# Performance work log

Hardware: AMD Instinct MI355X
Metric: run time of the kernel (lower is better)

Reference implementation:

```python
import jax, jax.numpy as jnp
import numpy as np

N = 100_000       # nodes
E = 1_600_000     # edges
G = 128           # graphs in batch
RAW_ND, RAW_ED = 9, 3
ND, ED, H = 16, 2, 32  # node_dim, edge_dim, GAT hidden (heads=1)


def _p(key, shape, scale=0.1):
    return jax.random.normal(key, shape, dtype=jnp.float32) * scale


def setup_inputs() -> dict:
    key = jax.random.key(0)
    ks = jax.random.split(key, 32)
    inp = {
        "node_feat": jax.random.normal(ks[0], (N, RAW_ND), dtype=jnp.float32),
        "edge_index": jax.random.randint(ks[1], (2, E), 0, N, dtype=jnp.int64)
        if jax.config.jax_enable_x64 else jax.random.randint(ks[1], (2, E), 0, N).astype(jnp.int32),
        "edge_attr": jax.random.normal(ks[2], (E, RAW_ED), dtype=jnp.float32),
        "batch": jnp.sort(jax.random.randint(ks[3], (N,), 0, G)).astype(jnp.int32),
        # encoders
        "W_ne": _p(ks[4], (RAW_ND, ND)), "b_ne": jnp.zeros((ND,), jnp.float32),
        "W_ee": _p(ks[5], (RAW_ED, ED)), "b_ee": jnp.zeros((ED,), jnp.float32),
        # readout
        "W_l3": _p(ks[6], (3 * H, 1)), "b_l3": jnp.zeros((1,), jnp.float32),
    }
    dims_in = [ND, H, H]
    for i in range(3):
        k = jax.random.split(ks[7 + i], 6)
        inp[f"W{i}"] = _p(k[0], (dims_in[i], H))
        inp[f"as{i}"] = _p(k[1], (H,))
        inp[f"ad{i}"] = _p(k[2], (H,))
        inp[f"We{i}"] = _p(k[3], (ED, H))
        inp[f"ae{i}"] = _p(k[4], (H,))
        inp[f"bb{i}"] = jnp.zeros((H,), jnp.float32)
    return inp


def _segment_softmax(logits, seg, num_segments):
    m = jax.ops.segment_max(logits, seg, num_segments=num_segments)
    m = jnp.where(jnp.isfinite(m), m, 0.0)
    e = jnp.exp(logits - m[seg])
    s = jax.ops.segment_sum(e, seg, num_segments=num_segments)
    return e / (s[seg] + 1e-16)


def _gat(x, src, dst, ef, W, a_s, a_d, We, a_e, b):
    # PyG GATConv, heads=1, negative_slope=0.2
    h = x @ W                                   # [N', H]
    a_src = h @ a_s                             # [N']
    a_dst = h @ a_d
    a_edge = (ef @ We) @ a_e                    # [E']
    logits = jax.nn.leaky_relu(a_src[src] + a_dst[dst] + a_edge, 0.2)
    att = _segment_softmax(logits, dst, h.shape[0])
    out = jax.ops.segment_sum(h[src] * att[:, None], dst, num_segments=h.shape[0])
    return out + b


def reference(node_feat, edge_index, edge_attr, batch,
              W_ne, b_ne, W_ee, b_ee, W_l3, b_l3,
              W0, as0, ad0, We0, ae0, bb0,
              W1, as1, ad1, We1, ae1, bb1,
              W2, as2, ad2, We2, ae2, bb2):
    n = node_feat.shape[0]
    x = node_feat @ W_ne + b_ne                 # NodeEncoder -> [N,16]
    ef = edge_attr @ W_ee + b_ee                # EdgeEncoder -> [E,2]
    # add_self_loops=True with fill_value='mean' (PyG default when edge_dim set)
    loop = jnp.arange(n, dtype=edge_index.dtype)
    src = jnp.concatenate([edge_index[0], loop])
    dst = jnp.concatenate([edge_index[1], loop])
    ef_fill = jnp.broadcast_to(ef.mean(axis=0), (n, ef.shape[1]))
    ef_aug = jnp.concatenate([ef, ef_fill], axis=0)
    x1 = _gat(x, src, dst, ef_aug, W0, as0, ad0, We0, ae0, bb0)
    x2 = _gat(x1, src, dst, ef_aug, W1, as1, ad1, We1, ae1, bb1)
    x3 = _gat(x2, src, dst, ef_aug, W2, as2, ad2, We2, ae2, bb2)
    x_cat = jnp.concatenate([x1, x2, x3], axis=1)  # [N, 96]
    sums = jax.ops.segment_sum(x_cat, batch, num_segments=G)
    cnt = jax.ops.segment_sum(jnp.ones((n,), x_cat.dtype), batch, num_segments=G)
    pooled = sums / jnp.maximum(cnt, 1.0)[:, None]   # global mean pool [G,96]
    return pooled @ W_l3 + b_l3                      # [G,1]
```

## Files before the change

kernel.cpp:

```cpp
#include <hip/hip_runtime.h>
#include <hip/hip_fp16.h>


#define NBUCK_SHIFT 8
#define NBUCK_MAX 512
#define CAP 6144
#define SLF_BIT 0x00800000u

__global__ void k_pre(const int* __restrict__ ei1, int* __restrict__ bucket_cnt,
                      const int* __restrict__ batch, int* __restrict__ bounds,
                      const float* __restrict__ Wne, const float* __restrict__ bne,
                      const float* __restrict__ W0, float* __restrict__ wf,
                      int n, int e, int ep, int nbH) {
    int b = blockIdx.x, t = threadIdx.x;
    if (b < nbH) {
        __shared__ int lh[NBUCK_MAX];
        lh[t] = 0; lh[t + 256] = 0;
        __syncthreads();
        int base = b * 4096;
#pragma unroll
        for (int i = 0; i < 16; ++i) {
            int gid = base + i * 256 + t;
            if (gid < ep) {
                int d = (gid < e) ? ei1[gid] : gid - e;
                atomicAdd(&lh[d >> NBUCK_SHIFT], 1);
            }
        }
        __syncthreads();
        if (lh[t]) atomicAdd(&bucket_cnt[t], lh[t]);
        if (lh[t + 256]) atomicAdd(&bucket_cnt[t + 256], lh[t + 256]);
        return;
    }
    for (int i = t; i < 288; i += 256) {
        int m = i >> 5, j = i & 31;
        float a = 0.f;
        for (int k = 0; k < 16; ++k) a += Wne[m * 16 + k] * W0[k * 32 + j];
        wf[i] = a;
    }
    if (t < 32) {
        float a = 0.f;
        for (int k = 0; k < 16; ++k) a += bne[k] * W0[k * 32 + t];
        wf[288 + t] = a;
    }
    for (int g = t; g <= 128; g += 256) {
        if (g == 128) { bounds[128] = n; continue; }
        int lo = 0, hi = n;
        while (lo < hi) {
            int mid = (lo + hi) >> 1;
            if (batch[mid] < g) lo = mid + 1; else hi = mid;
        }
        bounds[g] = lo;
    }
}

__global__ void k_hproj0(const float* __restrict__ nf, const float* __restrict__ wf,
                         const float* __restrict__ as_, const float* __restrict__ ad_,
                         unsigned int* __restrict__ h2, float* __restrict__ asrc,
                         float* __restrict__ adst, int n) {
    int node = blockIdx.x * 8 + (threadIdx.x >> 5);
    int j = threadIdx.x & 31;
    if (node >= n) return;
    const float* xr = nf + node * 9;
    float acc = wf[288 + j];
#pragma unroll
    for (int m = 0; m < 9; ++m) acc += xr[m] * wf[m * 32 + j];
    float accp = __shfl_down(acc, 1, 32);
    if ((j & 1) == 0) {
        __half2 hh = __floats2half2_rn(acc, accp);
        h2[(size_t)node * 16 + (j >> 1)] = *reinterpret_cast<unsigned int*>(&hh);
    }
    float r1 = acc * as_[j], r2 = acc * ad_[j];
#pragma unroll
    for (int off = 16; off > 0; off >>= 1) {
        r1 += __shfl_xor(r1, off, 32);
        r2 += __shfl_xor(r2, off, 32);
    }
    if (j == 0) { asrc[node] = r1; adst[node] = r2; }
}

__device__ __forceinline__ float2 h2f2u(unsigned int hw) {
    __half2 hh = *reinterpret_cast<__half2*>(&hw);
    return make_float2(__low2float(hh), __high2float(hh));
}

__global__ void k_hproj(const unsigned int* __restrict__ xh, const float* __restrict__ W,
                        const float* __restrict__ as_, const float* __restrict__ ad_,
                        unsigned int* __restrict__ h2, float* __restrict__ asrc,
                        float* __restrict__ adst, int n) {
    __shared__ float sW[1024];
    for (int i = threadIdx.x; i < 1024; i += 256) sW[i] = W[i];
    __syncthreads();
    int node = blockIdx.x * 8 + (threadIdx.x >> 5);
    int j = threadIdx.x & 31;
    if (node >= n) return;
    const unsigned int* xr = xh + (size_t)node * 16;
    float acc = 0.f;
#pragma unroll
    for (int w = 0; w < 16; ++w) {
        float2 f = h2f2u(xr[w]);
        acc += f.x * sW[(2 * w) * 32 + j] + f.y * sW[(2 * w + 1) * 32 + j];
    }
    float accp = __shfl_down(acc, 1, 32);
    if ((j & 1) == 0) {
        __half2 hh = __floats2half2_rn(acc, accp);
        h2[(size_t)node * 16 + (j >> 1)] = *reinterpret_cast<unsigned int*>(&hh);
    }
    float r1 = acc * as_[j], r2 = acc * ad_[j];
#pragma unroll
    for (int off = 16; off > 0; off >>= 1) {
        r1 += __shfl_xor(r1, off, 32);
        r2 += __shfl_xor(r2, off, 32);
    }
    if (j == 0) { asrc[node] = r1; adst[node] = r2; }
}

__global__ void __launch_bounds__(512)
k_scan(const int* __restrict__ bucket_cnt, int* __restrict__ bucket_base,
       int* __restrict__ bcursor, int nbuck, int ep, int* __restrict__ rp, int n) {
    __shared__ int s[512];
    int t = threadIdx.x;
    int v = (t < nbuck) ? bucket_cnt[t] : 0;
    s[t] = v;
    __syncthreads();
    for (int o = 1; o < 512; o <<= 1) {
        int x = (t >= o) ? s[t - o] : 0;
        __syncthreads();
        s[t] += x;
        __syncthreads();
    }
    int ex = s[t] - v;
    if (t < nbuck) { bucket_base[t] = ex; bcursor[t] = ex; }
    if (t == 0) { bucket_base[nbuck] = ep; rp[n] = ep; }
}

__global__ void k_binB(const int* __restrict__ ei0, const int* __restrict__ ei1,
                       const float* __restrict__ ea, const float* __restrict__ We,
                       const float* __restrict__ be, int* __restrict__ bcursor,
                       uint2* __restrict__ st, float2* __restrict__ partial,
                       int e, int ep) {
    __shared__ int lh[NBUCK_MAX], lcur[NBUCK_MAX];
    int t = threadIdx.x;
    lh[t] = 0; lh[t + 256] = 0;
    __syncthreads();
    int base = blockIdx.x * 4096;
    unsigned int sd[16], fh[16];
    int bk[16];
    float w00 = We[0], w10 = We[2], w20 = We[4];
    float w01 = We[1], w11 = We[3], w21 = We[5];
    float b0 = be[0], b1 = be[1];
    float cs0 = 0.f, cs1 = 0.f;
#pragma unroll
    for (int i = 0; i < 16; ++i) {
        int gid = base + i * 256 + t;
        bk[i] = -1;
        if (gid < ep) {
            int s, d;
            if (gid < e) {
                s = ei0[gid]; d = ei1[gid];
                const float* r = ea + (size_t)gid * 3;
                float a0 = r[0], a1 = r[1], a2 = r[2];
                float f0 = a0 * w00 + a1 * w10 + a2 * w20 + b0;
                float f1 = a0 * w01 + a1 * w11 + a2 * w21 + b1;
                cs0 += f0; cs1 += f1;
                sd[i] = ((unsigned int)s << NBUCK_SHIFT) | (unsigned int)(d & 255);
                __half2 hh = __floats2half2_rn(f0, f1);
                fh[i] = *reinterpret_cast<unsigned int*>(&hh);
            } else {
                s = d = gid - e;
                sd[i] = 0x80000000u | ((unsigned int)s << NBUCK_SHIFT)
                      | (unsigned int)(d & 255);
                fh[i] = 0;
            }
            bk[i] = d >> NBUCK_SHIFT;
            atomicAdd(&lh[bk[i]], 1);
        }
    }
#pragma unroll
    for (int off = 32; off > 0; off >>= 1) {
        cs0 += __shfl_xor(cs0, off, 64);
        cs1 += __shfl_xor(cs1, off, 64);
    }
    if ((t & 63) == 0)
        partial[(blockIdx.x << 2) + (t >> 6)] = make_float2(cs0, cs1);
    __syncthreads();
    if (lh[t] > 0) lcur[t] = atomicAdd(&bcursor[t], lh[t]);
    if (lh[t + 256] > 0) lcur[t + 256] = atomicAdd(&bcursor[t + 256], lh[t + 256]);
    __syncthreads();
#pragma unroll
    for (int i = 0; i < 16; ++i) {
        if (bk[i] >= 0) {
            int pos = atomicAdd(&lcur[bk[i]], 1);
            st[pos] = make_uint2(sd[i], fh[i]);
        }
    }
}

__global__ void __launch_bounds__(512)
k_binC(const uint2* __restrict__ st, const int* __restrict__ bucket_base,
       int* __restrict__ rp, uint2* __restrict__ rec, int n, int nbuck,
       const float* __restrict__ We0, const float* __restrict__ ae0,
       const float* __restrict__ We1, const float* __restrict__ ae1,
       const float* __restrict__ We2, const float* __restrict__ ae2,
       const float2* __restrict__ partial, int nw, float einv,
       float* __restrict__ consts) {
    int k = blockIdx.x, t = threadIdx.x;
    if (k == nbuck) {
        __shared__ float r0[512], r1[512];
        float m0 = 0.f, m1 = 0.f;
        for (int i = t; i < nw; i += 512) {
            float2 v = partial[i];
            m0 += v.x; m1 += v.y;
        }
        r0[t] = m0; r1[t] = m1;
        __syncthreads();
        for (int o = 256; o > 0; o >>= 1) {
            if (t < o) { r0[t] += r0[t + o]; r1[t] += r1[t + o]; }
            __syncthreads();
        }
        if (t == 0) {
            float fm0 = r0[0] * einv, fm1 = r1[0] * einv;
            const float* We[3] = {We0, We1, We2};
            const float* ae[3] = {ae0, ae1, ae2};
            for (int l = 0; l < 3; ++l) {
                float c0 = 0.f, c1 = 0.f;
                for (int j = 0; j < 32; ++j) {
                    c0 += We[l][j] * ae[l][j];
                    c1 += We[l][32 + j] * ae[l][j];
                }
                consts[l * 2 + 0] = c0;
                consts[l * 2 + 1] = c1;
                consts[6 + l] = fm0 * c0 + fm1 * c1;
            }
        }
        return;
    }
    __shared__ int nh[256], ns[256];
    __shared__ uint2 rs[CAP];
    int s0 = bucket_base[k], s1 = bucket_base[k + 1];
    int cnt = s1 - s0;
    uint2 lv[12];
    if (t < 256) nh[t] = 0;
    __syncthreads();
#pragma unroll
    for (int u = 0; u < 12; ++u) {
        int i = s0 + u * 512 + t;
        if (i < s1) {
            uint2 v = st[i];
            lv[u] = v;
            atomicAdd(&nh[v.x & 255], 1);
        }
    }
    __syncthreads();
    if (t < 256) ns[t] = nh[t];
    __syncthreads();
    for (int o = 1; o < 256; o <<= 1) {
        int add = 0;
        if (t < 256 && t >= o) add = ns[t - o];
        __syncthreads();
        if (t < 256) ns[t] += add;
        __syncthreads();
    }
    int node0 = k << NBUCK_SHIFT;
    if (t < 256) {
        int startl = ns[t] - nh[t];
        if (node0 + t < n) rp[node0 + t] = s0 + startl;
        nh[t] = startl;
    }
    __syncthreads();
#pragma unroll
    for (int u = 0; u < 12; ++u) {
        int i = s0 + u * 512 + t;
        if (i < s1) {
            uint2 v = lv[u];
            int pos = atomicAdd(&nh[v.x & 255], 1);
            uint2 r = make_uint2(v.x >> NBUCK_SHIFT, v.y);
            if (pos < CAP) rs[pos] = r;
            else rec[s0 + pos] = r;
        }
    }
    __syncthreads();
    int m = cnt < CAP ? cnt : CAP;
    for (int i = t; i < m; i += 512)
        rec[s0 + i] = rs[i];
}

__device__ __forceinline__ void agg_step(const unsigned int* __restrict__ h2,
                                         const uint2* ed, int t, int sub, int woff,
                                         float& a0, float& a1, float& a2, float& a3) {
    uint2 sp = ed[t + sub];
    float p4 = __uint_as_float(sp.y);
    uint2 hv = *reinterpret_cast<const uint2*>(h2 + (((int)sp.x << 4) + woff));
    __half2 hlo = *reinterpret_cast<__half2*>(&hv.x);
    __half2 hhi = *reinterpret_cast<__half2*>(&hv.y);
    a0 = fmaf(__low2float(hlo), p4, a0);
    a1 = fmaf(__high2float(hlo), p4, a1);
    a2 = fmaf(__low2float(hhi), p4, a2);
    a3 = fmaf(__high2float(hhi), p4, a3);
}

template <bool STORE_X>
__global__ void k_agg(const int* __restrict__ rp, const uint2* __restrict__ rec,
                      const float* __restrict__ asrc, const float* __restrict__ adst,
                      const float* __restrict__ consts, const unsigned int* __restrict__ h2,
                      const float* __restrict__ bb, unsigned int* __restrict__ xout,
                      const float* __restrict__ wl3, float* __restrict__ vout,
                      int n, int layer) {
    __shared__ uint2 sed[8][32];
    int g = threadIdx.x >> 5;
    int j = threadIdx.x & 31;
    int sub = j >> 3;
    int q = j & 7;
    int woff = q << 1;
    float c0 = consts[layer * 2], c1 = consts[layer * 2 + 1];
    float loopc = consts[6 + layer];
    float4 bb4 = reinterpret_cast<const float4*>(bb)[q];
    float4 wl34 = reinterpret_cast<const float4*>(wl3)[q];
    uint2* ed = sed[g];
    int stride = gridDim.x * 8;
    for (int node = blockIdx.x * 8 + g; node < n; node += stride) {
        int r0 = rp[node], r1 = rp[node + 1];
        float adn = adst[node];
        float a0 = 0.f, a1 = 0.f, a2 = 0.f, a3 = 0.f, psum = 0.f;
        for (int c = r0; c < r1; c += 32) {
            int i = c + j;
            float pe = 0.f; unsigned int s = 0;
            if (i < r1) {
                unsigned long long rv = *reinterpret_cast<const unsigned long long*>(
                    rec + i);
                unsigned int sx = (unsigned int)rv;
                s = sx & 0x7fffffu;
                unsigned int fv = (unsigned int)(rv >> 32);
                __half2 hh = *reinterpret_cast<__half2*>(&fv);
                float ae = (sx & SLF_BIT) ? loopc
                         : fmaf(__low2float(hh), c0, __high2float(hh) * c1);
                float lg = asrc[s] + adn + ae;
                lg = lg > 0.f ? lg : 0.2f * lg;
                pe = __expf(lg);
            }
            psum += pe;
            ed[j] = make_uint2(s, __float_as_uint(pe));
            int cnt = min(32, r1 - c);
            int t = 0;
            for (; t + 8 <= cnt; t += 8) {
                agg_step(h2, ed, t, sub, woff, a0, a1, a2, a3);
                agg_step(h2, ed, t + 4, sub, woff, a0, a1, a2, a3);
            }
            if (t < cnt) { agg_step(h2, ed, t, sub, woff, a0, a1, a2, a3); t += 4; }
            if (t < cnt) { agg_step(h2, ed, t, sub, woff, a0, a1, a2, a3); }
        }
        a0 += __shfl_xor(a0, 8, 32);  a0 += __shfl_xor(a0, 16, 32);
        a1 += __shfl_xor(a1, 8, 32);  a1 += __shfl_xor(a1, 16, 32);
        a2 += __shfl_xor(a2, 8, 32);  a2 += __shfl_xor(a2, 16, 32);
        a3 += __shfl_xor(a3, 8, 32);  a3 += __shfl_xor(a3, 16, 32);
#pragma unroll
        for (int off = 16; off > 0; off >>= 1) psum += __shfl_xor(psum, off, 32);
        float inv = __builtin_amdgcn_rcpf(psum + 1e-16f);
        float r0v = fmaf(a0, inv, bb4.x);
        float r1v = fmaf(a1, inv, bb4.y);
        float r2v = fmaf(a2, inv, bb4.z);
        float r3v = fmaf(a3, inv, bb4.w);
        if (STORE_X) {
            if (sub == 0) {
                __half2 lo = __floats2half2_rn(r0v, r1v);
                __half2 hi = __floats2half2_rn(r2v, r3v);
                uint2 wv = make_uint2(*reinterpret_cast<unsigned int*>(&lo),
                                      *reinterpret_cast<unsigned int*>(&hi));
                reinterpret_cast<uint2*>(xout)[(size_t)node * 8 + q] = wv;
            }
        }
        float v = r0v * wl34.x + r1v * wl34.y + r2v * wl34.z + r3v * wl34.w;
        v += __shfl_xor(v, 1, 32);
        v += __shfl_xor(v, 2, 32);
        v += __shfl_xor(v, 4, 32);
        if (j == 0) vout[node] = v;
    }
}

__global__ void k_dotv(const float* __restrict__ v0, const float* __restrict__ v1,
                       const float* __restrict__ v2, const int* __restrict__ bounds,
                       const float* __restrict__ bl3, float* __restrict__ out) {
    __shared__ float red[256];
    int g = blockIdx.x, t = threadIdx.x;
    int s0 = bounds[g], s1 = bounds[g + 1];
    float acc = 0.f;
    for (int i = s0 + t; i < s1; i += 256) acc += v0[i] + v1[i] + v2[i];
    red[t] = acc;
    __syncthreads();
    for (int o = 128; o > 0; o >>= 1) {
        if (t < o) red[t] += red[t + o];
        __syncthreads();
    }
    if (t == 0) {
        float c = (float)(s1 - s0);
        if (c < 1.f) c = 1.f;
        out[g] = red[0] / c + bl3[0];
    }
}

extern "C" void kernel_launch(void* const* d_in, const int* in_sizes, int n_in,
                              void* d_out, int out_size, void* d_ws, size_t ws_size,
                              hipStream_t stream) {
    (void)n_in; (void)out_size; (void)ws_size;
    const float* nf    = (const float*)d_in[0];
    const int*   ei    = (const int*)d_in[1];
    const float* ea    = (const float*)d_in[2];
    const int*   batch = (const int*)d_in[3];
    const float* W_ne  = (const float*)d_in[4];
    const float* b_ne  = (const float*)d_in[5];
    const float* W_ee  = (const float*)d_in[6];
    const float* b_ee  = (const float*)d_in[7];
    const float* W_l3  = (const float*)d_in[8];
    const float* b_l3  = (const float*)d_in[9];
    const float *Wl[3], *asl[3], *adl[3], *Wel[3], *ael[3], *bbl[3];
    for (int l = 0; l < 3; ++l) {
        Wl[l]  = (const float*)d_in[10 + 6 * l];
        asl[l] = (const float*)d_in[11 + 6 * l];
        adl[l] = (const float*)d_in[12 + 6 * l];
        Wel[l] = (const float*)d_in[13 + 6 * l];
        ael[l] = (const float*)d_in[14 + 6 * l];
        bbl[l] = (const float*)d_in[15 + 6 * l];
    }

    const int n  = in_sizes[3];
    const int e  = in_sizes[2] / 3;
    const int ep = e + n;
    const int* ei0 = ei;
    const int* ei1 = ei + e;
    const int nbuck = (n + 255) >> NBUCK_SHIFT;

    char* w = (char*)d_ws;
    size_t off = 0;
    auto alloc = [&](size_t b) { size_t o = off; off = (off + b + 255) & ~(size_t)255; return o; };
    unsigned int* x1h     = (unsigned int*)(w + alloc((size_t)n * 16 * 4));
    unsigned int* x2h     = (unsigned int*)(w + alloc((size_t)n * 16 * 4));
    unsigned int* h2a     = (unsigned int*)(w + alloc((size_t)n * 16 * 4));
    unsigned int* h2b     = (unsigned int*)(w + alloc((size_t)n * 16 * 4));
    float*        asrcA   = (float*)(w + alloc((size_t)n * 4));
    float*        adstA   = (float*)(w + alloc((size_t)n * 4));
    float*        asrcB   = (float*)(w + alloc((size_t)n * 4));
    float*        adstB   = (float*)(w + alloc((size_t)n * 4));
    float*        v0      = (float*)(w + alloc((size_t)n * 4));
    float*        v1      = (float*)(w + alloc((size_t)n * 4));
    float*        v2      = (float*)(w + alloc((size_t)n * 4));
    uint2*        st      = (uint2*)(w + alloc((size_t)ep * 8));
    uint2*        rec     = (uint2*)(w + alloc((size_t)ep * 8));
    int*          rp      = (int*)(w + alloc((size_t)(n + 1) * 4));
    int*          bcnt    = (int*)(w + alloc(NBUCK_MAX * 4));
    int*          bbase   = (int*)(w + alloc((NBUCK_MAX + 1) * 4));
    int*          bcur    = (int*)(w + alloc(NBUCK_MAX * 4));
    float2*       partial = (float2*)(w + alloc((size_t)8192 * 8));
    float*        consts  = (float*)(w + alloc(256));
    int*          bounds  = (int*)(w + alloc(129 * 4));
    float*        wfbuf   = (float*)(w + alloc(320 * 4));

    hipMemsetAsync(bcnt, 0, NBUCK_MAX * 4, stream);

    int nbH = (ep + 4095) / 4096;
    int nw  = nbH * 4;
    int nbN = (n + 7) / 8;
    int nbA = 2048;

    k_pre<<<nbH + 1, 256, 0, stream>>>(ei1, bcnt, batch, bounds,
                                       W_ne, b_ne, Wl[0], wfbuf, n, e, ep, nbH);
    k_hproj0<<<nbN, 256, 0, stream>>>(nf, wfbuf, asl[0], adl[0],
                                      h2a, asrcA, adstA, n);
    k_scan<<<1, 512, 0, stream>>>(bcnt, bbase, bcur, nbuck, ep, rp, n);
    k_binB<<<nbH, 256, 0, stream>>>(ei0, ei1, ea, W_ee, b_ee, bcur, st,
                                    partial, e, ep);
    k_binC<<<nbuck + 1, 512, 0, stream>>>(st, bbase, rp, rec, n, nbuck,
                                          Wel[0], ael[0], Wel[1], ael[1],
                                          Wel[2], ael[2], partial, nw,
                                          1.0f / (float)e, consts);

    k_agg<true><<<nbA, 256, 0, stream>>>(rp, rec, asrcA, adstA, consts, h2a,
                                         bbl[0], x1h, W_l3 + 0, v0, n, 0);
    k_hproj<<<nbN, 256, 0, stream>>>(x1h, Wl[1], asl[1], adl[1], h2b, asrcB, adstB, n);
    k_agg<true><<<nbA, 256, 0, stream>>>(rp, rec, asrcB, adstB, consts, h2b,
                                         bbl[1], x2h, W_l3 + 32, v1, n, 1);
    k_hproj<<<nbN, 256, 0, stream>>>(x2h, Wl[2], asl[2], adl[2], h2a, asrcA, adstA, n);
    k_agg<false><<<nbA, 256, 0, stream>>>(rp, rec, asrcA, adstA, consts, h2a,
                                          bbl[2], nullptr, W_l3 + 64, v2, n, 2);
    k_dotv<<<128, 256, 0, stream>>>(v0, v1, v2, bounds, b_l3, (float*)d_out);
}
```

Measured before the change: 312.2 us.

## Recompute source attention scores from gathered features instead of gathering asrc

Stops precomputing and storing per-node a_src in the projection kernels. The aggregation kernel now computes each edge's source score as a dot product of the already-gathered fp16 h row with a_s, using an 8-lane shuffle reduction, and fuses the softmax exp into the per-edge gather loop. This removes one random 4-byte gather per edge and the asrc writes, in exchange for extra shuffles and FMAs per edge. It also drops the 2x unroll of the gather loop and marks padding slots with an invalid bit, which can lower memory-level parallelism.

```diff
diff --git a/kernel.cpp b/kernel.cpp
--- a/kernel.cpp
+++ b/kernel.cpp
@@ -6,6 +6,7 @@
 #define NBUCK_MAX 512
 #define CAP 6144
 #define SLF_BIT 0x00800000u
+#define INV_BIT 0x01000000u
 
 __global__ void k_pre(const int* __restrict__ ei1, int* __restrict__ bucket_cnt,
                       const int* __restrict__ batch, int* __restrict__ bounds,
@@ -54,8 +55,8 @@
 }
 
 __global__ void k_hproj0(const float* __restrict__ nf, const float* __restrict__ wf,
-                         const float* __restrict__ as_, const float* __restrict__ ad_,
-                         unsigned int* __restrict__ h2, float* __restrict__ asrc,
+                         const float* __restrict__ ad_,
+                         unsigned int* __restrict__ h2,
                          float* __restrict__ adst, int n) {
     int node = blockIdx.x * 8 + (threadIdx.x >> 5);
     int j = threadIdx.x & 31;
@@ -69,13 +70,11 @@
         __half2 hh = __floats2half2_rn(acc, accp);
         h2[(size_t)node * 16 + (j >> 1)] = *reinterpret_cast<unsigned int*>(&hh);
     }
-    float r1 = acc * as_[j], r2 = acc * ad_[j];
-#pragma unroll
-    for (int off = 16; off > 0; off >>= 1) {
-        r1 += __shfl_xor(r1, off, 32);
+    float r2 = acc * ad_[j];
+#pragma unroll
+    for (int off = 16; off > 0; off >>= 1)
         r2 += __shfl_xor(r2, off, 32);
-    }
-    if (j == 0) { asrc[node] = r1; adst[node] = r2; }
+    if (j == 0) adst[node] = r2;
 }
 
 __device__ __forceinline__ float2 h2f2u(unsigned int hw) {
@@ -84,8 +83,8 @@
 }
 
 __global__ void k_hproj(const unsigned int* __restrict__ xh, const float* __restrict__ W,
-                        const float* __restrict__ as_, const float* __restrict__ ad_,
-                        unsigned int* __restrict__ h2, float* __restrict__ asrc,
+                        const float* __restrict__ ad_,
+                        unsigned int* __restrict__ h2,
                         float* __restrict__ adst, int n) {
     __shared__ float sW[1024];
     for (int i = threadIdx.x; i < 1024; i += 256) sW[i] = W[i];
@@ -105,13 +104,11 @@
         __half2 hh = __floats2half2_rn(acc, accp);
         h2[(size_t)node * 16 + (j >> 1)] = *reinterpret_cast<unsigned int*>(&hh);
     }
-    float r1 = acc * as_[j], r2 = acc * ad_[j];
-#pragma unroll
-    for (int off = 16; off > 0; off >>= 1) {
-        r1 += __shfl_xor(r1, off, 32);
+    float r2 = acc * ad_[j];
+#pragma unroll
+    for (int off = 16; off > 0; off >>= 1)
         r2 += __shfl_xor(r2, off, 32);
-    }
-    if (j == 0) { asrc[node] = r1; adst[node] = r2; }
+    if (j == 0) adst[node] = r2;
 }
 
 __global__ void __launch_bounds__(512)
@@ -284,26 +281,13 @@
         rec[s0 + i] = rs[i];
 }
 
-__device__ __forceinline__ void agg_step(const unsigned int* __restrict__ h2,
-                                         const uint2* ed, int t, int sub, int woff,
-                                         float& a0, float& a1, float& a2, float& a3) {
-    uint2 sp = ed[t + sub];
-    float p4 = __uint_as_float(sp.y);
-    uint2 hv = *reinterpret_cast<const uint2*>(h2 + (((int)sp.x << 4) + woff));
-    __half2 hlo = *reinterpret_cast<__half2*>(&hv.x);
-    __half2 hhi = *reinterpret_cast<__half2*>(&hv.y);
-    a0 = fmaf(__low2float(hlo), p4, a0);
-    a1 = fmaf(__high2float(hlo), p4, a1);
-    a2 = fmaf(__low2float(hhi), p4, a2);
-    a3 = fmaf(__high2float(hhi), p4, a3);
-}
-
 template <bool STORE_X>
 __global__ void k_agg(const int* __restrict__ rp, const uint2* __restrict__ rec,
-                      const float* __restrict__ asrc, const float* __restrict__ adst,
+                      const float* __restrict__ adst,
                       const float* __restrict__ consts, const unsigned int* __restrict__ h2,
                       const float* __restrict__ bb, unsigned int* __restrict__ xout,
                       const float* __restrict__ wl3, float* __restrict__ vout,
+                      const float* __restrict__ as_,
                       int n, int layer) {
     __shared__ uint2 sed[8][32];
     int g = threadIdx.x >> 5;
@@ -315,6 +299,7 @@
     float loopc = consts[6 + layer];
     float4 bb4 = reinterpret_cast<const float4*>(bb)[q];
     float4 wl34 = reinterpret_cast<const float4*>(wl3)[q];
+    float4 as4 = reinterpret_cast<const float4*>(as_)[q];
     uint2* ed = sed[g];
     int stride = gridDim.x * 8;
     for (int node = blockIdx.x * 8 + g; node < n; node += stride) {
@@ -323,37 +308,48 @@
         float a0 = 0.f, a1 = 0.f, a2 = 0.f, a3 = 0.f, psum = 0.f;
         for (int c = r0; c < r1; c += 32) {
             int i = c + j;
-            float pe = 0.f; unsigned int s = 0;
-            if (i < r1) {
-                unsigned long long rv = *reinterpret_cast<const unsigned long long*>(
-                    rec + i);
-                unsigned int sx = (unsigned int)rv;
-                s = sx & 0x7fffffu;
-                unsigned int fv = (unsigned int)(rv >> 32);
-                __half2 hh = *reinterpret_cast<__half2*>(&fv);
+            uint2 rv = make_uint2(INV_BIT, 0);
+            if (i < r1)
+                rv = *reinterpret_cast<const uint2*>(rec + i);
+            ed[j] = rv;
+            int cnt = min(32, r1 - c);
+            for (int t = 0; t < cnt; t += 4) {
+                uint2 sp = ed[t + sub];
+                unsigned int sx = sp.x;
+                int s = (int)(sx & 0x7fffffu);
+                uint2 hv = *reinterpret_cast<const uint2*>(h2 + ((s << 4) + woff));
+                __half2 hlo = *reinterpret_cast<__half2*>(&hv.x);
+                __half2 hhi = *reinterpret_cast<__half2*>(&hv.y);
+                float h0 = __low2float(hlo), h1 = __high2float(hlo);
+                float h2v = __low2float(hhi), h3 = __high2float(hhi);
+                float dp = h0 * as4.x;
+                dp = fmaf(h1, as4.y, dp);
+                dp = fmaf(h2v, as4.z, dp);
+                dp = fmaf(h3, as4.w, dp);
+                dp += __shfl_xor(dp, 1, 32);
+                dp += __shfl_xor(dp, 2, 32);
+                dp += __shfl_xor(dp, 4, 32);
+                unsigned int fv = sp.y;
+                __half2 fh = *reinterpret_cast<__half2*>(&fv);
                 float ae = (sx & SLF_BIT) ? loopc
-                         : fmaf(__low2float(hh), c0, __high2float(hh) * c1);
-                float lg = asrc[s] + adn + ae;
+                         : fmaf(__low2float(fh), c0, __high2float(fh) * c1);
+                float lg = dp + adn + ae;
                 lg = lg > 0.f ? lg : 0.2f * lg;
-                pe = __expf(lg);
+                float pe = __expf(lg);
+                if (sx & INV_BIT) pe = 0.f;
+                psum += pe;
+                a0 = fmaf(h0, pe, a0);
+                a1 = fmaf(h1, pe, a1);
+                a2 = fmaf(h2v, pe, a2);
+                a3 = fmaf(h3, pe, a3);
             }
-            psum += pe;
-            ed[j] = make_uint2(s, __float_as_uint(pe));
-            int cnt = min(32, r1 - c);
-            int t = 0;
-            for (; t + 8 <= cnt; t += 8) {
-                agg_step(h2, ed, t, sub, woff, a0, a1, a2, a3);
-                agg_step(h2, ed, t + 4, sub, woff, a0, a1, a2, a3);
-            }
-            if (t < cnt) { agg_step(h2, ed, t, sub, woff, a0, a1, a2, a3); t += 4; }
-            if (t < cnt) { agg_step(h2, ed, t, sub, woff, a0, a1, a2, a3); }
         }
         a0 += __shfl_xor(a0, 8, 32);  a0 += __shfl_xor(a0, 16, 32);
         a1 += __shfl_xor(a1, 8, 32);  a1 += __shfl_xor(a1, 16, 32);
         a2 += __shfl_xor(a2, 8, 32);  a2 += __shfl_xor(a2, 16, 32);
         a3 += __shfl_xor(a3, 8, 32);  a3 += __shfl_xor(a3, 16, 32);
-#pragma unroll
-        for (int off = 16; off > 0; off >>= 1) psum += __shfl_xor(psum, off, 32);
+        psum += __shfl_xor(psum, 8, 32);
+        psum += __shfl_xor(psum, 16, 32);
         float inv = __builtin_amdgcn_rcpf(psum + 1e-16f);
         float r0v = fmaf(a0, inv, bb4.x);
         float r1v = fmaf(a1, inv, bb4.y);
@@ -435,9 +431,7 @@
     unsigned int* x2h     = (unsigned int*)(w + alloc((size_t)n * 16 * 4));
     unsigned int* h2a     = (unsigned int*)(w + alloc((size_t)n * 16 * 4));
     unsigned int* h2b     = (unsigned int*)(w + alloc((size_t)n * 16 * 4));
-    float*        asrcA   = (float*)(w + alloc((size_t)n * 4));
     float*        adstA   = (float*)(w + alloc((size_t)n * 4));
-    float*        asrcB   = (float*)(w + alloc((size_t)n * 4));
     float*        adstB   = (float*)(w + alloc((size_t)n * 4));
     float*        v0      = (float*)(w + alloc((size_t)n * 4));
     float*        v1      = (float*)(w + alloc((size_t)n * 4));
@@ -462,8 +456,7 @@
 
     k_pre<<<nbH + 1, 256, 0, stream>>>(ei1, bcnt, batch, bounds,
                                        W_ne, b_ne, Wl[0], wfbuf, n, e, ep, nbH);
-    k_hproj0<<<nbN, 256, 0, stream>>>(nf, wfbuf, asl[0], adl[0],
-                                      h2a, asrcA, adstA, n);
+    k_hproj0<<<nbN, 256, 0, stream>>>(nf, wfbuf, adl[0], h2a, adstA, n);
     k_scan<<<1, 512, 0, stream>>>(bcnt, bbase, bcur, nbuck, ep, rp, n);
     k_binB<<<nbH, 256, 0, stream>>>(ei0, ei1, ea, W_ee, b_ee, bcur, st,
                                     partial, e, ep);
@@ -472,13 +465,13 @@
                                           Wel[2], ael[2], partial, nw,
                                           1.0f / (float)e, consts);
 
-    k_agg<true><<<nbA, 256, 0, stream>>>(rp, rec, asrcA, adstA, consts, h2a,
-                                         bbl[0], x1h, W_l3 + 0, v0, n, 0);
-    k_hproj<<<nbN, 256, 0, stream>>>(x1h, Wl[1], asl[1], adl[1], h2b, asrcB, adstB, n);
-    k_agg<true><<<nbA, 256, 0, stream>>>(rp, rec, asrcB, adstB, consts, h2b,
-                                         bbl[1], x2h, W_l3 + 32, v1, n, 1);
-    k_hproj<<<nbN, 256, 0, stream>>>(x2h, Wl[2], asl[2], adl[2], h2a, asrcA, adstA, n);
-    k_agg<false><<<nbA, 256, 0, stream>>>(rp, rec, asrcA, adstA, consts, h2a,
-                                          bbl[2], nullptr, W_l3 + 64, v2, n, 2);
+    k_agg<true><<<nbA, 256, 0, stream>>>(rp, rec, adstA, consts, h2a,
+                                         bbl[0], x1h, W_l3 + 0, v0, asl[0], n, 0);
+    k_hproj<<<nbN, 256, 0, stream>>>(x1h, Wl[1], adl[1], h2b, adstB, n);
+    k_agg<true><<<nbA, 256, 0, stream>>>(rp, rec, adstB, consts, h2b,
+                                         bbl[1], x2h, W_l3 + 32, v1, asl[1], n, 1);
+    k_hproj<<<nbN, 256, 0, stream>>>(x2h, Wl[2], adl[2], h2a, adstA, n);
+    k_agg<false><<<nbA, 256, 0, stream>>>(rp, rec, adstA, consts, h2a,
+                                          bbl[2], nullptr, W_l3 + 64, v2, asl[2], n, 2);
     k_dotv<<<128, 256, 0, stream>>>(v0, v1, v2, bounds, b_l3, (float*)d_out);
 }
```

Measured after the change: 321.2 us. 2.9% more time.

## Fuse GAT layer tail into one persistent cooperative kernel with grid syncs

Applied to the files above, without the earlier changes.

Replaces the seven separate launches for the projection, aggregation and pooling stages with a single cooperative kernel that runs all three GAT layers and the readout, separated by grid-wide barriers. The hproj0 stage is moved after binning into the fused tail. The aim is to remove per-launch overhead and the drain/refill gaps between small kernels. In exchange, grid syncs add their own cost, the block count is capped by occupancy, and the projection stages switch to grid-stride loops over fewer blocks. The old multi-launch path is kept as a fallback.

```diff
diff --git a/kernel.cpp b/kernel.cpp
--- a/kernel.cpp
+++ b/kernel.cpp
@@ -1,5 +1,8 @@
 #include <hip/hip_runtime.h>
 #include <hip/hip_fp16.h>
+#include <hip/hip_cooperative_groups.h>
+
+namespace cg = cooperative_groups;
 
 
 #define NBUCK_SHIFT 8
@@ -53,235 +56,74 @@
     }
 }
 
-__global__ void k_hproj0(const float* __restrict__ nf, const float* __restrict__ wf,
-                         const float* __restrict__ as_, const float* __restrict__ ad_,
-                         unsigned int* __restrict__ h2, float* __restrict__ asrc,
-                         float* __restrict__ adst, int n) {
-    int node = blockIdx.x * 8 + (threadIdx.x >> 5);
-    int j = threadIdx.x & 31;
-    if (node >= n) return;
-    const float* xr = nf + node * 9;
-    float acc = wf[288 + j];
-#pragma unroll
-    for (int m = 0; m < 9; ++m) acc += xr[m] * wf[m * 32 + j];
-    float accp = __shfl_down(acc, 1, 32);
-    if ((j & 1) == 0) {
-        __half2 hh = __floats2half2_rn(acc, accp);
-        h2[(size_t)node * 16 + (j >> 1)] = *reinterpret_cast<unsigned int*>(&hh);
-    }
-    float r1 = acc * as_[j], r2 = acc * ad_[j];
-#pragma unroll
-    for (int off = 16; off > 0; off >>= 1) {
-        r1 += __shfl_xor(r1, off, 32);
-        r2 += __shfl_xor(r2, off, 32);
-    }
-    if (j == 0) { asrc[node] = r1; adst[node] = r2; }
-}
-
 __device__ __forceinline__ float2 h2f2u(unsigned int hw) {
     __half2 hh = *reinterpret_cast<__half2*>(&hw);
     return make_float2(__low2float(hh), __high2float(hh));
 }
 
-__global__ void k_hproj(const unsigned int* __restrict__ xh, const float* __restrict__ W,
-                        const float* __restrict__ as_, const float* __restrict__ ad_,
-                        unsigned int* __restrict__ h2, float* __restrict__ asrc,
-                        float* __restrict__ adst, int n) {
-    __shared__ float sW[1024];
+
+__device__ __forceinline__ void body_hproj0(const float* __restrict__ nf,
+                                            const float* __restrict__ wf,
+                                            const float* __restrict__ as_,
+                                            const float* __restrict__ ad_,
+                                            unsigned int* __restrict__ h2,
+                                            float* __restrict__ asrc,
+                                            float* __restrict__ adst, int n) {
+    int g = threadIdx.x >> 5, j = threadIdx.x & 31;
+    int stride = gridDim.x * 8;
+    for (int node = blockIdx.x * 8 + g; node < n; node += stride) {
+        const float* xr = nf + node * 9;
+        float acc = wf[288 + j];
+#pragma unroll
+        for (int m = 0; m < 9; ++m) acc += xr[m] * wf[m * 32 + j];
+        float accp = __shfl_down(acc, 1, 32);
+        if ((j & 1) == 0) {
+            __half2 hh = __floats2half2_rn(acc, accp);
+            h2[(size_t)node * 16 + (j >> 1)] = *reinterpret_cast<unsigned int*>(&hh);
+        }
+        float r1 = acc * as_[j], r2 = acc * ad_[j];
+#pragma unroll
+        for (int off = 16; off > 0; off >>= 1) {
+            r1 += __shfl_xor(r1, off, 32);
+            r2 += __shfl_xor(r2, off, 32);
+        }
+        if (j == 0) { asrc[node] = r1; adst[node] = r2; }
+    }
+}
+
+__device__ __forceinline__ void body_hproj(float* sW,
+                                           const unsigned int* __restrict__ xh,
+                                           const float* __restrict__ W,
+                                           const float* __restrict__ as_,
+                                           const float* __restrict__ ad_,
+                                           unsigned int* __restrict__ h2,
+                                           float* __restrict__ asrc,
+                                           float* __restrict__ adst, int n) {
     for (int i = threadIdx.x; i < 1024; i += 256) sW[i] = W[i];
     __syncthreads();
-    int node = blockIdx.x * 8 + (threadIdx.x >> 5);
-    int j = threadIdx.x & 31;
-    if (node >= n) return;
-    const unsigned int* xr = xh + (size_t)node * 16;
-    float acc = 0.f;
-#pragma unroll
-    for (int w = 0; w < 16; ++w) {
-        float2 f = h2f2u(xr[w]);
-        acc += f.x * sW[(2 * w) * 32 + j] + f.y * sW[(2 * w + 1) * 32 + j];
-    }
-    float accp = __shfl_down(acc, 1, 32);
-    if ((j & 1) == 0) {
-        __half2 hh = __floats2half2_rn(acc, accp);
-        h2[(size_t)node * 16 + (j >> 1)] = *reinterpret_cast<unsigned int*>(&hh);
-    }
-    float r1 = acc * as_[j], r2 = acc * ad_[j];
-#pragma unroll
-    for (int off = 16; off > 0; off >>= 1) {
-        r1 += __shfl_xor(r1, off, 32);
-        r2 += __shfl_xor(r2, off, 32);
-    }
-    if (j == 0) { asrc[node] = r1; adst[node] = r2; }
-}
-
-__global__ void __launch_bounds__(512)
-k_scan(const int* __restrict__ bucket_cnt, int* __restrict__ bucket_base,
-       int* __restrict__ bcursor, int nbuck, int ep, int* __restrict__ rp, int n) {
-    __shared__ int s[512];
-    int t = threadIdx.x;
-    int v = (t < nbuck) ? bucket_cnt[t] : 0;
-    s[t] = v;
-    __syncthreads();
-    for (int o = 1; o < 512; o <<= 1) {
-        int x = (t >= o) ? s[t - o] : 0;
-        __syncthreads();
-        s[t] += x;
-        __syncthreads();
-    }
-    int ex = s[t] - v;
-    if (t < nbuck) { bucket_base[t] = ex; bcursor[t] = ex; }
-    if (t == 0) { bucket_base[nbuck] = ep; rp[n] = ep; }
-}
-
-__global__ void k_binB(const int* __restrict__ ei0, const int* __restrict__ ei1,
-                       const float* __restrict__ ea, const float* __restrict__ We,
-                       const float* __restrict__ be, int* __restrict__ bcursor,
-                       uint2* __restrict__ st, float2* __restrict__ partial,
-                       int e, int ep) {
-    __shared__ int lh[NBUCK_MAX], lcur[NBUCK_MAX];
-    int t = threadIdx.x;
-    lh[t] = 0; lh[t + 256] = 0;
-    __syncthreads();
-    int base = blockIdx.x * 4096;
-    unsigned int sd[16], fh[16];
-    int bk[16];
-    float w00 = We[0], w10 = We[2], w20 = We[4];
-    float w01 = We[1], w11 = We[3], w21 = We[5];
-    float b0 = be[0], b1 = be[1];
-    float cs0 = 0.f, cs1 = 0.f;
-#pragma unroll
-    for (int i = 0; i < 16; ++i) {
-        int gid = base + i * 256 + t;
-        bk[i] = -1;
-        if (gid < ep) {
-            int s, d;
-            if (gid < e) {
-                s = ei0[gid]; d = ei1[gid];
-                const float* r = ea + (size_t)gid * 3;
-                float a0 = r[0], a1 = r[1], a2 = r[2];
-                float f0 = a0 * w00 + a1 * w10 + a2 * w20 + b0;
-                float f1 = a0 * w01 + a1 * w11 + a2 * w21 + b1;
-                cs0 += f0; cs1 += f1;
-                sd[i] = ((unsigned int)s << NBUCK_SHIFT) | (unsigned int)(d & 255);
-                __half2 hh = __floats2half2_rn(f0, f1);
-                fh[i] = *reinterpret_cast<unsigned int*>(&hh);
-            } else {
-                s = d = gid - e;
-                sd[i] = 0x80000000u | ((unsigned int)s << NBUCK_SHIFT)
-                      | (unsigned int)(d & 255);
-                fh[i] = 0;
-            }
-            bk[i] = d >> NBUCK_SHIFT;
-            atomicAdd(&lh[bk[i]], 1);
-        }
-    }
-#pragma unroll
-    for (int off = 32; off > 0; off >>= 1) {
-        cs0 += __shfl_xor(cs0, off, 64);
-        cs1 += __shfl_xor(cs1, off, 64);
-    }
-    if ((t & 63) == 0)
-        partial[(blockIdx.x << 2) + (t >> 6)] = make_float2(cs0, cs1);
-    __syncthreads();
-    if (lh[t] > 0) lcur[t] = atomicAdd(&bcursor[t], lh[t]);
-    if (lh[t + 256] > 0) lcur[t + 256] = atomicAdd(&bcursor[t + 256], lh[t + 256]);
-    __syncthreads();
-#pragma unroll
-    for (int i = 0; i < 16; ++i) {
-        if (bk[i] >= 0) {
-            int pos = atomicAdd(&lcur[bk[i]], 1);
-            st[pos] = make_uint2(sd[i], fh[i]);
-        }
-    }
-}
-
-__global__ void __launch_bounds__(512)
-k_binC(const uint2* __restrict__ st, const int* __restrict__ bucket_base,
-       int* __restrict__ rp, uint2* __restrict__ rec, int n, int nbuck,
-       const float* __restrict__ We0, const float* __restrict__ ae0,
-       const float* __restrict__ We1, const float* __restrict__ ae1,
-       const float* __restrict__ We2, const float* __restrict__ ae2,
-       const float2* __restrict__ partial, int nw, float einv,
-       float* __restrict__ consts) {
-    int k = blockIdx.x, t = threadIdx.x;
-    if (k == nbuck) {
-        __shared__ float r0[512], r1[512];
-        float m0 = 0.f, m1 = 0.f;
-        for (int i = t; i < nw; i += 512) {
-            float2 v = partial[i];
-            m0 += v.x; m1 += v.y;
-        }
-        r0[t] = m0; r1[t] = m1;
-        __syncthreads();
-        for (int o = 256; o > 0; o >>= 1) {
-            if (t < o) { r0[t] += r0[t + o]; r1[t] += r1[t + o]; }
-            __syncthreads();
-        }
-        if (t == 0) {
-            float fm0 = r0[0] * einv, fm1 = r1[0] * einv;
-            const float* We[3] = {We0, We1, We2};
-            const float* ae[3] = {ae0, ae1, ae2};
-            for (int l = 0; l < 3; ++l) {
-                float c0 = 0.f, c1 = 0.f;
-                for (int j = 0; j < 32; ++j) {
-                    c0 += We[l][j] * ae[l][j];
-                    c1 += We[l][32 + j] * ae[l][j];
-                }
-                consts[l * 2 + 0] = c0;
-                consts[l * 2 + 1] = c1;
-                consts[6 + l] = fm0 * c0 + fm1 * c1;
-            }
-        }
-        return;
-    }
-    __shared__ int nh[256], ns[256];
-    __shared__ uint2 rs[CAP];
-    int s0 = bucket_base[k], s1 = bucket_base[k + 1];
-    int cnt = s1 - s0;
-    uint2 lv[12];
-    if (t < 256) nh[t] = 0;
-    __syncthreads();
-#pragma unroll
-    for (int u = 0; u < 12; ++u) {
-        int i = s0 + u * 512 + t;
-        if (i < s1) {
-            uint2 v = st[i];
-            lv[u] = v;
-            atomicAdd(&nh[v.x & 255], 1);
-        }
-    }
-    __syncthreads();
-    if (t < 256) ns[t] = nh[t];
-    __syncthreads();
-    for (int o = 1; o < 256; o <<= 1) {
-        int add = 0;
-        if (t < 256 && t >= o) add = ns[t - o];
-        __syncthreads();
-        if (t < 256) ns[t] += add;
-        __syncthreads();
-    }
-    int node0 = k << NBUCK_SHIFT;
-    if (t < 256) {
-        int startl = ns[t] - nh[t];
-        if (node0 + t < n) rp[node0 + t] = s0 + startl;
-        nh[t] = startl;
-    }
-    __syncthreads();
-#pragma unroll
-    for (int u = 0; u < 12; ++u) {
-        int i = s0 + u * 512 + t;
-        if (i < s1) {
-            uint2 v = lv[u];
-            int pos = atomicAdd(&nh[v.x & 255], 1);
-            uint2 r = make_uint2(v.x >> NBUCK_SHIFT, v.y);
-            if (pos < CAP) rs[pos] = r;
-            else rec[s0 + pos] = r;
-        }
-    }
-    __syncthreads();
-    int m = cnt < CAP ? cnt : CAP;
-    for (int i = t; i < m; i += 512)
-        rec[s0 + i] = rs[i];
+    int g = threadIdx.x >> 5, j = threadIdx.x & 31;
+    int stride = gridDim.x * 8;
+    for (int node = blockIdx.x * 8 + g; node < n; node += stride) {
+        const unsigned int* xr = xh + (size_t)node * 16;
+        float acc = 0.f;
+#pragma unroll
+        for (int w = 0; w < 16; ++w) {
+            float2 f = h2f2u(xr[w]);
+            acc += f.x * sW[(2 * w) * 32 + j] + f.y * sW[(2 * w + 1) * 32 + j];
+        }
+        float accp = __shfl_down(acc, 1, 32);
+        if ((j & 1) == 0) {
+            __half2 hh = __floats2half2_rn(acc, accp);
+            h2[(size_t)node * 16 + (j >> 1)] = *reinterpret_cast<unsigned int*>(&hh);
+        }
+        float r1 = acc * as_[j], r2 = acc * ad_[j];
+#pragma unroll
+        for (int off = 16; off > 0; off >>= 1) {
+            r1 += __shfl_xor(r1, off, 32);
+            r2 += __shfl_xor(r2, off, 32);
+        }
+        if (j == 0) { asrc[node] = r1; adst[node] = r2; }
+    }
 }
 
 __device__ __forceinline__ void agg_step(const unsigned int* __restrict__ h2,
@@ -298,14 +140,18 @@
     a3 = fmaf(__high2float(hhi), p4, a3);
 }
 
-template <bool STORE_X>
-__global__ void k_agg(const int* __restrict__ rp, const uint2* __restrict__ rec,
-                      const float* __restrict__ asrc, const float* __restrict__ adst,
-                      const float* __restrict__ consts, const unsigned int* __restrict__ h2,
-                      const float* __restrict__ bb, unsigned int* __restrict__ xout,
-                      const float* __restrict__ wl3, float* __restrict__ vout,
-                      int n, int layer) {
-    __shared__ uint2 sed[8][32];
+__device__ __forceinline__ void body_agg(uint2* sedbase,
+                                         const int* __restrict__ rp,
+                                         const uint2* __restrict__ rec,
+                                         const float* __restrict__ asrc,
+                                         const float* __restrict__ adst,
+                                         const float* __restrict__ consts,
+                                         const unsigned int* __restrict__ h2,
+                                         const float* __restrict__ bb,
+                                         unsigned int* __restrict__ xout,
+                                         const float* __restrict__ wl3,
+                                         float* __restrict__ vout,
+                                         int n, int layer, bool store_x) {
     int g = threadIdx.x >> 5;
     int j = threadIdx.x & 31;
     int sub = j >> 3;
@@ -315,7 +161,7 @@
     float loopc = consts[6 + layer];
     float4 bb4 = reinterpret_cast<const float4*>(bb)[q];
     float4 wl34 = reinterpret_cast<const float4*>(wl3)[q];
-    uint2* ed = sed[g];
+    uint2* ed = sedbase + g * 32;
     int stride = gridDim.x * 8;
     for (int node = blockIdx.x * 8 + g; node < n; node += stride) {
         int r0 = rp[node], r1 = rp[node + 1];
@@ -359,14 +205,12 @@
         float r1v = fmaf(a1, inv, bb4.y);
         float r2v = fmaf(a2, inv, bb4.z);
         float r3v = fmaf(a3, inv, bb4.w);
-        if (STORE_X) {
-            if (sub == 0) {
-                __half2 lo = __floats2half2_rn(r0v, r1v);
-                __half2 hi = __floats2half2_rn(r2v, r3v);
-                uint2 wv = make_uint2(*reinterpret_cast<unsigned int*>(&lo),
-                                      *reinterpret_cast<unsigned int*>(&hi));
-                reinterpret_cast<uint2*>(xout)[(size_t)node * 8 + q] = wv;
-            }
+        if (store_x && sub == 0) {
+            __half2 lo = __floats2half2_rn(r0v, r1v);
+            __half2 hi = __floats2half2_rn(r2v, r3v);
+            uint2 wv = make_uint2(*reinterpret_cast<unsigned int*>(&lo),
+                                  *reinterpret_cast<unsigned int*>(&hi));
+            reinterpret_cast<uint2*>(xout)[(size_t)node * 8 + q] = wv;
         }
         float v = r0v * wl34.x + r1v * wl34.y + r2v * wl34.z + r3v * wl34.w;
         v += __shfl_xor(v, 1, 32);
@@ -376,11 +220,15 @@
     }
 }
 
-__global__ void k_dotv(const float* __restrict__ v0, const float* __restrict__ v1,
-                       const float* __restrict__ v2, const int* __restrict__ bounds,
-                       const float* __restrict__ bl3, float* __restrict__ out) {
-    __shared__ float red[256];
+__device__ __forceinline__ void body_dotv(float* red,
+                                          const float* __restrict__ v0,
+                                          const float* __restrict__ v1,
+                                          const float* __restrict__ v2,
+                                          const int* __restrict__ bounds,
+                                          const float* __restrict__ bl3,
+                                          float* __restrict__ out) {
     int g = blockIdx.x, t = threadIdx.x;
+    if (g >= 128) return;
     int s0 = bounds[g], s1 = bounds[g + 1];
     float acc = 0.f;
     for (int i = s0 + t; i < s1; i += 256) acc += v0[i] + v1[i] + v2[i];
@@ -395,6 +243,242 @@
         if (c < 1.f) c = 1.f;
         out[g] = red[0] / c + bl3[0];
     }
+}
+
+__global__ void k_hproj0(const float* nf, const float* wf, const float* as_,
+                         const float* ad_, unsigned int* h2, float* asrc,
+                         float* adst, int n) {
+    body_hproj0(nf, wf, as_, ad_, h2, asrc, adst, n);
+}
+
+__global__ void k_hproj(const unsigned int* xh, const float* W, const float* as_,
+                        const float* ad_, unsigned int* h2, float* asrc,
+                        float* adst, int n) {
+    __shared__ float sW[1024];
+    body_hproj(sW, xh, W, as_, ad_, h2, asrc, adst, n);
+}
+
+__global__ void k_agg(const int* rp, const uint2* rec, const float* asrc,
+                      const float* adst, const float* consts,
+                      const unsigned int* h2, const float* bb,
+                      unsigned int* xout, const float* wl3, float* vout,
+                      int n, int layer, int store_x) {
+    __shared__ uint2 sed[256];
+    body_agg(sed, rp, rec, asrc, adst, consts, h2, bb, xout, wl3, vout,
+             n, layer, store_x != 0);
+}
+
+__global__ void k_dotv(const float* v0, const float* v1, const float* v2,
+                       const int* bounds, const float* bl3, float* out) {
+    __shared__ float red[256];
+    body_dotv(red, v0, v1, v2, bounds, bl3, out);
+}
+
+struct TailArgs {
+    const int* rp; const uint2* rec;
+    const float* nf; const float* wf;
+    unsigned int *h2a, *h2b, *x1h, *x2h;
+    float *asrcA, *adstA, *asrcB, *adstB;
+    const float* consts;
+    const float *W1, *W2;
+    const float *as0, *ad0, *as1, *ad1, *as2, *ad2;
+    const float *bb0, *bb1, *bb2;
+    const float* wl3;
+    float *v0, *v1, *v2;
+    const int* bounds; const float* bl3; float* out;
+    int n;
+};
+
+__global__ void __launch_bounds__(256)
+k_tail(TailArgs a) {
+    __shared__ float smem[1024];
+    cg::grid_group grid = cg::this_grid();
+    body_hproj0(a.nf, a.wf, a.as0, a.ad0, a.h2a, a.asrcA, a.adstA, a.n);
+    grid.sync();
+    body_agg((uint2*)smem, a.rp, a.rec, a.asrcA, a.adstA, a.consts, a.h2a,
+             a.bb0, a.x1h, a.wl3 + 0, a.v0, a.n, 0, true);
+    grid.sync();
+    body_hproj(smem, a.x1h, a.W1, a.as1, a.ad1, a.h2b, a.asrcB, a.adstB, a.n);
+    grid.sync();
+    body_agg((uint2*)smem, a.rp, a.rec, a.asrcB, a.adstB, a.consts, a.h2b,
+             a.bb1, a.x2h, a.wl3 + 32, a.v1, a.n, 1, true);
+    grid.sync();
+    body_hproj(smem, a.x2h, a.W2, a.as2, a.ad2, a.h2a, a.asrcA, a.adstA, a.n);
+    grid.sync();
+    body_agg((uint2*)smem, a.rp, a.rec, a.asrcA, a.adstA, a.consts, a.h2a,
+             a.bb2, nullptr, a.wl3 + 64, a.v2, a.n, 2, false);
+    grid.sync();
+    body_dotv(smem, a.v0, a.v1, a.v2, a.bounds, a.bl3, a.out);
+}
+
+__global__ void __launch_bounds__(512)
+k_scan(const int* __restrict__ bucket_cnt, int* __restrict__ bucket_base,
+       int* __restrict__ bcursor, int nbuck, int ep, int* __restrict__ rp, int n) {
+    __shared__ int s[512];
+    int t = threadIdx.x;
+    int v = (t < nbuck) ? bucket_cnt[t] : 0;
+    s[t] = v;
+    __syncthreads();
+    for (int o = 1; o < 512; o <<= 1) {
+        int x = (t >= o) ? s[t - o] : 0;
+        __syncthreads();
+        s[t] += x;
+        __syncthreads();
+    }
+    int ex = s[t] - v;
+    if (t < nbuck) { bucket_base[t] = ex; bcursor[t] = ex; }
+    if (t == 0) { bucket_base[nbuck] = ep; rp[n] = ep; }
+}
+
+__global__ void k_binB(const int* __restrict__ ei0, const int* __restrict__ ei1,
+                       const float* __restrict__ ea, const float* __restrict__ We,
+                       const float* __restrict__ be, int* __restrict__ bcursor,
+                       uint2* __restrict__ st, float2* __restrict__ partial,
+                       int e, int ep) {
+    __shared__ int lh[NBUCK_MAX], lcur[NBUCK_MAX];
+    int t = threadIdx.x;
+    lh[t] = 0; lh[t + 256] = 0;
+    __syncthreads();
+    int base = blockIdx.x * 4096;
+    unsigned int sd[16], fh[16];
+    int bk[16];
+    float w00 = We[0], w10 = We[2], w20 = We[4];
+    float w01 = We[1], w11 = We[3], w21 = We[5];
+    float b0 = be[0], b1 = be[1];
+    float cs0 = 0.f, cs1 = 0.f;
+#pragma unroll
+    for (int i = 0; i < 16; ++i) {
+        int gid = base + i * 256 + t;
+        bk[i] = -1;
+        if (gid < ep) {
+            int s, d;
+            if (gid < e) {
+                s = ei0[gid]; d = ei1[gid];
+                const float* r = ea + (size_t)gid * 3;
+                float a0 = r[0], a1 = r[1], a2 = r[2];
+                float f0 = a0 * w00 + a1 * w10 + a2 * w20 + b0;
+                float f1 = a0 * w01 + a1 * w11 + a2 * w21 + b1;
+                cs0 += f0; cs1 += f1;
+                sd[i] = ((unsigned int)s << NBUCK_SHIFT) | (unsigned int)(d & 255);
+                __half2 hh = __floats2half2_rn(f0, f1);
+                fh[i] = *reinterpret_cast<unsigned int*>(&hh);
+            } else {
+                s = d = gid - e;
+                sd[i] = 0x80000000u | ((unsigned int)s << NBUCK_SHIFT)
+                      | (unsigned int)(d & 255);
+                fh[i] = 0;
+            }
+            bk[i] = d >> NBUCK_SHIFT;
+            atomicAdd(&lh[bk[i]], 1);
+        }
+    }
+#pragma unroll
+    for (int off = 32; off > 0; off >>= 1) {
+        cs0 += __shfl_xor(cs0, off, 64);
+        cs1 += __shfl_xor(cs1, off, 64);
+    }
+    if ((t & 63) == 0)
+        partial[(blockIdx.x << 2) + (t >> 6)] = make_float2(cs0, cs1);
+    __syncthreads();
+    if (lh[t] > 0) lcur[t] = atomicAdd(&bcursor[t], lh[t]);
+    if (lh[t + 256] > 0) lcur[t + 256] = atomicAdd(&bcursor[t + 256], lh[t + 256]);
+    __syncthreads();
+#pragma unroll
+    for (int i = 0; i < 16; ++i) {
+        if (bk[i] >= 0) {
+            int pos = atomicAdd(&lcur[bk[i]], 1);
+            st[pos] = make_uint2(sd[i], fh[i]);
+        }
+    }
+}
+
+__global__ void __launch_bounds__(512)
+k_binC(const uint2* __restrict__ st, const int* __restrict__ bucket_base,
+       int* __restrict__ rp, uint2* __restrict__ rec, int n, int nbuck,
+       const float* __restrict__ We0, const float* __restrict__ ae0,
+       const float* __restrict__ We1, const float* __restrict__ ae1,
+       const float* __restrict__ We2, const float* __restrict__ ae2,
+       const float2* __restrict__ partial, int nw, float einv,
+       float* __restrict__ consts) {
+    int k = blockIdx.x, t = threadIdx.x;
+    if (k == nbuck) {
+        __shared__ float r0[512], r1[512];
+        float m0 = 0.f, m1 = 0.f;
+        for (int i = t; i < nw; i += 512) {
+            float2 v = partial[i];
+            m0 += v.x; m1 += v.y;
+        }
+        r0[t] = m0; r1[t] = m1;
+        __syncthreads();
+        for (int o = 256; o > 0; o >>= 1) {
+            if (t < o) { r0[t] += r0[t + o]; r1[t] += r1[t + o]; }
+            __syncthreads();
+        }
+        if (t == 0) {
+            float fm0 = r0[0] * einv, fm1 = r1[0] * einv;
+            const float* We[3] = {We0, We1, We2};
+            const float* ae[3] = {ae0, ae1, ae2};
+            for (int l = 0; l < 3; ++l) {
+                float c0 = 0.f, c1 = 0.f;
+                for (int j = 0; j < 32; ++j) {
+                    c0 += We[l][j] * ae[l][j];
+                    c1 += We[l][32 + j] * ae[l][j];
+                }
+                consts[l * 2 + 0] = c0;
+                consts[l * 2 + 1] = c1;
+                consts[6 + l] = fm0 * c0 + fm1 * c1;
+            }
+        }
+        return;
+    }
+    __shared__ int nh[256], ns[256];
+    __shared__ uint2 rs[CAP];
+    int s0 = bucket_base[k], s1 = bucket_base[k + 1];
+    int cnt = s1 - s0;
+    uint2 lv[12];
+    if (t < 256) nh[t] = 0;
+    __syncthreads();
+#pragma unroll
+    for (int u = 0; u < 12; ++u) {
+        int i = s0 + u * 512 + t;
+        if (i < s1) {
+            uint2 v = st[i];
+            lv[u] = v;
+            atomicAdd(&nh[v.x & 255], 1);
+        }
+    }
+    __syncthreads();
+    if (t < 256) ns[t] = nh[t];
+    __syncthreads();
+    for (int o = 1; o < 256; o <<= 1) {
+        int add = 0;
+        if (t < 256 && t >= o) add = ns[t - o];
+        __syncthreads();
+        if (t < 256) ns[t] += add;
+        __syncthreads();
+    }
+    int node0 = k << NBUCK_SHIFT;
+    if (t < 256) {
+        int startl = ns[t] - nh[t];
+        if (node0 + t < n) rp[node0 + t] = s0 + startl;
+        nh[t] = startl;
+    }
+    __syncthreads();
+#pragma unroll
+    for (int u = 0; u < 12; ++u) {
+        int i = s0 + u * 512 + t;
+        if (i < s1) {
+            uint2 v = lv[u];
+            int pos = atomicAdd(&nh[v.x & 255], 1);
+            uint2 r = make_uint2(v.x >> NBUCK_SHIFT, v.y);
+            if (pos < CAP) rs[pos] = r;
+            else rec[s0 + pos] = r;
+        }
+    }
+    __syncthreads();
+    int m = cnt < CAP ? cnt : CAP;
+    for (int i = t; i < m; i += 512)
+        rec[s0 + i] = rs[i];
 }
 
 extern "C" void kernel_launch(void* const* d_in, const int* in_sizes, int n_in,
@@ -458,12 +542,9 @@
     int nbH = (ep + 4095) / 4096;
     int nw  = nbH * 4;
     int nbN = (n + 7) / 8;
-    int nbA = 2048;
 
     k_pre<<<nbH + 1, 256, 0, stream>>>(ei1, bcnt, batch, bounds,
                                        W_ne, b_ne, Wl[0], wfbuf, n, e, ep, nbH);
-    k_hproj0<<<nbN, 256, 0, stream>>>(nf, wfbuf, asl[0], adl[0],
-                                      h2a, asrcA, adstA, n);
     k_scan<<<1, 512, 0, stream>>>(bcnt, bbase, bcur, nbuck, ep, rp, n);
     k_binB<<<nbH, 256, 0, stream>>>(ei0, ei1, ea, W_ee, b_ee, bcur, st,
                                     partial, e, ep);
@@ -472,13 +553,53 @@
                                           Wel[2], ael[2], partial, nw,
                                           1.0f / (float)e, consts);
 
-    k_agg<true><<<nbA, 256, 0, stream>>>(rp, rec, asrcA, adstA, consts, h2a,
-                                         bbl[0], x1h, W_l3 + 0, v0, n, 0);
-    k_hproj<<<nbN, 256, 0, stream>>>(x1h, Wl[1], asl[1], adl[1], h2b, asrcB, adstB, n);
-    k_agg<true><<<nbA, 256, 0, stream>>>(rp, rec, asrcB, adstB, consts, h2b,
-                                         bbl[1], x2h, W_l3 + 32, v1, n, 1);
-    k_hproj<<<nbN, 256, 0, stream>>>(x2h, Wl[2], asl[2], adl[2], h2a, asrcA, adstA, n);
-    k_agg<false><<<nbA, 256, 0, stream>>>(rp, rec, asrcA, adstA, consts, h2a,
-                                          bbl[2], nullptr, W_l3 + 64, v2, n, 2);
-    k_dotv<<<128, 256, 0, stream>>>(v0, v1, v2, bounds, b_l3, (float*)d_out);
-}
+    static int coopBlocks = -2;
+    if (coopBlocks == -2) {
+        int dev = 0;
+        hipGetDevice(&dev);
+        int cuCount = 0, coopSup = 0, perCU = 0;
+        hipDeviceGetAttribute(&cuCount, hipDeviceAttributeMultiprocessorCount, dev);
+        hipDeviceGetAttribute(&coopSup, hipDeviceAttributeCooperativeLaunch, dev);
+        hipError_t oe = hipOccupancyMaxActiveBlocksPerMultiprocessor(
+            &perCU, k_tail, 256, 0);
+        int cap = (oe == hipSuccess && coopSup) ? perCU * cuCount : 0;
+        coopBlocks = (cap >= 512) ? (cap < 2048 ? cap : 2048) : -1;
+    }
+
+    bool coopDone = false;
+    if (coopBlocks > 0) {
+        TailArgs ta;
+        ta.rp = rp; ta.rec = rec; ta.nf = nf; ta.wf = wfbuf;
+        ta.h2a = h2a; ta.h2b = h2b; ta.x1h = x1h; ta.x2h = x2h;
+        ta.asrcA = asrcA; ta.adstA = adstA; ta.asrcB = asrcB; ta.adstB = adstB;
+        ta.consts = consts; ta.W1 = Wl[1]; ta.W2 = Wl[2];
+        ta.as0 = asl[0]; ta.ad0 = adl[0];
+        ta.as1 = asl[1]; ta.ad1 = adl[1];
+        ta.as2 = asl[2]; ta.ad2 = adl[2];
+        ta.bb0 = bbl[0]; ta.bb1 = bbl[1]; ta.bb2 = bbl[2];
+        ta.wl3 = W_l3; ta.v0 = v0; ta.v1 = v1; ta.v2 = v2;
+        ta.bounds = bounds; ta.bl3 = b_l3; ta.out = (float*)d_out;
+        ta.n = n;
+        void* kargs[] = { &ta };
+        hipError_t le = hipLaunchCooperativeKernel(
+            (const void*)k_tail, dim3(coopBlocks), dim3(256), kargs, 0, stream);
+        if (le == hipSuccess) coopDone = true;
+        else { coopBlocks = -1; (void)hipGetLastError(); }
+    }
+    if (!coopDone) {
+        int nbA = 2048;
+        k_hproj0<<<nbN, 256, 0, stream>>>(nf, wfbuf, asl[0], adl[0],
+                                          h2a, asrcA, adstA, n);
+        k_agg<<<nbA, 256, 0, stream>>>(rp, rec, asrcA, adstA, consts, h2a,
+                                       bbl[0], x1h, W_l3 + 0, v0, n, 0, 1);
+        k_hproj<<<nbN, 256, 0, stream>>>(x1h, Wl[1], asl[1], adl[1],
+                                         h2b, asrcB, adstB, n);
+        k_agg<<<nbA, 256, 0, stream>>>(rp, rec, asrcB, adstB, consts, h2b,
+                                       bbl[1], x2h, W_l3 + 32, v1, n, 1, 1);
+        k_hproj<<<nbN, 256, 0, stream>>>(x2h, Wl[2], asl[2], adl[2],
+                                         h2a, asrcA, adstA, n);
+        k_agg<<<nbA, 256, 0, stream>>>(rp, rec, asrcA, adstA, consts, h2a,
+                                       bbl[2], nullptr, W_l3 + 64, v2, n, 2, 0);
+        k_dotv<<<128, 256, 0, stream>>>(v0, v1, v2, bounds, b_l3, (float*)d_out);
+    }
+}
```

Result: slower. 816.7 us (+161.6%).
